# Performance work log

Hardware: AMD Instinct MI355X
Metric: run time of the kernel (lower is better)

The kernel has to match this reference:

```python
import jax, jax.numpy as jnp
import numpy as np

N_NODES = {'movie': 50000, 'director': 10000, 'actor': 25000}
# relation name -> (src_type, dst_type, num_edges)
RELS = {'md': ('movie', 'director', 150000),
        'dm': ('director', 'movie', 150000),
        'ma': ('movie', 'actor', 300000),
        'am': ('actor', 'movie', 300000)}
F_IN, HID, HEADS, OUT = 1024, 256, 8, 4
HD = HID // HEADS  # 32 per-head dim


def setup_inputs() -> dict:
    key = jax.random.key(0)
    kit = iter(jax.random.split(key, 128))
    def nrm(shape, s):
        return jax.random.normal(next(kit), shape, jnp.float32) * s
    inp = {}
    for t, n in N_NODES.items():
        inp['x_' + t] = nrm((n, F_IN), 1.0)
    for rn, (st, dt, e) in RELS.items():
        inp['e_' + rn + '_src'] = jax.random.randint(next(kit), (e,), 0, N_NODES[st], dtype=jnp.int32)
        inp['e_' + rn + '_dst'] = jax.random.randint(next(kit), (e,), 0, N_NODES[dt], dtype=jnp.int32)
        inp['a_' + rn] = nrm((HEADS, HD, HD), 0.05)   # per-relation attention matrix
        inp['m_' + rn] = nrm((HEADS, HD, HD), 0.05)   # per-relation message matrix
        inp['p_' + rn] = jnp.ones((HEADS,), jnp.float32)  # relation priority
    for t in N_NODES:
        inp['W_in_' + t] = nrm((F_IN, HID), 0.02)
        inp['b_in_' + t] = jnp.zeros((HID,), jnp.float32)
        for nm in ('k', 'q', 'v'):
            inp['W' + nm + '_' + t] = nrm((HID, HID), 0.05)
            inp['b' + nm + '_' + t] = jnp.zeros((HID,), jnp.float32)
        inp['Wa_' + t] = nrm((HID, HID), 0.05)
        inp['ba_' + t] = jnp.zeros((HID,), jnp.float32)
        inp['skip_' + t] = jnp.array(1.0, jnp.float32)
    inp['W_out'] = nrm((HID, OUT), 0.05)
    inp['b_out'] = jnp.zeros((OUT,), jnp.float32)
    return inp


def _forward(p):
    # per-node-type input projection (the HGT.lin_dict step)
    h = {t: p['x_' + t] @ p['W_in_' + t] + p['b_in_' + t] for t in N_NODES}
    # per-type K/Q/V projections, reshaped to [N, H, D]
    def proj(nm):
        return {t: (h[t] @ p['W' + nm + '_' + t] + p['b' + nm + '_' + t]).reshape(-1, HEADS, HD)
                for t in N_NODES}
    k, q, v = proj('k'), proj('q'), proj('v')
    scale = 1.0 / np.sqrt(HD)
    # per-edge-type: gather, relation-transform, score
    buf = {t: [] for t in N_NODES}
    for rn, (st, dt, _) in RELS.items():
        si, di = p['e_' + rn + '_src'], p['e_' + rn + '_dst']
        ke = jnp.einsum('ehd,hdf->ehf', k[st][si], p['a_' + rn])  # [E,H,D]
        ve = jnp.einsum('ehd,hdf->ehf', v[st][si], p['m_' + rn])  # [E,H,D]
        al = (q[dt][di] * ke).sum(-1) * (p['p_' + rn] * scale)    # [E,H]
        buf[dt].append((di, al, ve))
    # destination-grouped segment softmax + scatter aggregation
    out = {}
    for t, n in N_NODES.items():
        di = jnp.concatenate([b[0] for b in buf[t]])
        al = jnp.concatenate([b[1] for b in buf[t]])
        ve = jnp.concatenate([b[2] for b in buf[t]])
        amax = jax.ops.segment_max(al, di, num_segments=n)        # [N,H]
        amax = jnp.where(jnp.isfinite(amax), amax, 0.0)
        ex = jnp.exp(al - amax[di])
        den = jax.ops.segment_sum(ex, di, num_segments=n)[di]
        w = ex / jnp.where(den > 0, den, 1.0)                     # [E,H]
        agg = jax.ops.segment_sum(w[:, :, None] * ve, di, num_segments=n).reshape(n, HID)
        o = jax.nn.gelu(agg @ p['Wa_' + t] + p['ba_' + t])
        beta = jax.nn.sigmoid(p['skip_' + t])                     # gated skip connection
        out[t] = beta * o + (1.0 - beta) * h[t]
    # final classifier on movie nodes
    return out['movie'] @ p['W_out'] + p['b_out']


def reference(x_movie, x_director, x_actor, e_md_src, e_md_dst, a_md, m_md, p_md, e_dm_src, e_dm_dst, a_dm, m_dm, p_dm, e_ma_src, e_ma_dst, a_ma, m_ma, p_ma, e_am_src, e_am_dst, a_am, m_am, p_am, W_in_movie, b_in_movie, Wk_movie, bk_movie, Wq_movie, bq_movie, Wv_movie, bv_movie, Wa_movie, ba_movie, skip_movie, W_in_director, b_in_director, Wk_director, bk_director, Wq_director, bq_director, Wv_director, bv_director, Wa_director, ba_director, skip_director, W_in_actor, b_in_actor, Wk_actor, bk_actor, Wq_actor, bq_actor, Wv_actor, bv_actor, Wa_actor, ba_actor, skip_actor, W_out, b_out):
    p = dict(locals())
    return _forward(p)
```

## Files before the change

kernel.cpp:

```cpp
#include <hip/hip_runtime.h>
#include <math.h>

#define NM 50000
#define ND 10000
#define NA 25000
#define E_DM 150000
#define E_AM 300000
#define E_TOT (E_DM + E_AM)
#define HID 256
#define HEADS 8
#define HD 32
#define FIN 1024
#define SCALE 0.17677669529663687f

typedef __attribute__((ext_vector_type(8))) short short8;
typedef __attribute__((ext_vector_type(4))) float f32x4;

typedef __attribute__((address_space(1))) const unsigned char gas_u8;
typedef __attribute__((address_space(3))) unsigned char las_u8;

__device__ __forceinline__ void gload16(const void* g, void* l) {
    gas_u8* gp = (gas_u8*)(unsigned long long)(uintptr_t)g;
    las_u8* lp = (las_u8*)(unsigned int)(uintptr_t)l;
    __builtin_amdgcn_global_load_lds((const __attribute__((address_space(1))) void*)gp,
                                     (__attribute__((address_space(3))) void*)lp, 16, 0, 0);
}

__device__ __forceinline__ unsigned int pk_bf16(float x, float y) {
    unsigned int a = __float_as_uint(x), b = __float_as_uint(y);
    a += 0x7FFFu + ((a >> 16) & 1u);
    b += 0x7FFFu + ((b >> 16) & 1u);
    return (a >> 16) | (b & 0xFFFF0000u);
}
__device__ __forceinline__ unsigned short to_bf16(float x) {
    unsigned int a = __float_as_uint(x);
    a += 0x7FFFu + ((a >> 16) & 1u);
    return (unsigned short)(a >> 16);
}
__device__ __forceinline__ float bf2f(unsigned short u) {
    return __uint_as_float(((unsigned int)u) << 16);
}

struct F4 { const float* W[4]; const float* b[4]; const float* a[4]; float* Wf[4]; float* bf[4]; };
__global__ void fold_w4(F4 f4) {
    int di = blockIdx.y;
    const float* W = f4.W[di]; const float* b = f4.b[di]; const float* a = f4.a[di];
    float* Wf = f4.Wf[di]; float* bf = f4.bf[di];
    int c = threadIdx.x;
    int h = c >> 5, f = c & 31;
    int r = blockIdx.x;
    float acc = 0.f;
    if (r < HID) {
        #pragma unroll
        for (int d = 0; d < HD; ++d)
            acc += W[r * HID + h * HD + d] * a[(h * HD + d) * HD + f];
        Wf[r * HID + c] = acc;
    } else {
        #pragma unroll
        for (int d = 0; d < HD; ++d)
            acc += b[h * HD + d] * a[(h * HD + d) * HD + f];
        bf[c] = acc;
    }
}

struct PDesc { const float* W; unsigned short* out; int K; int b0; };
struct PMulti { PDesc d[9]; int nd; };
__global__ void wt_pack(PMulti pm) {
    int bid = blockIdx.x; int di = 0;
    #pragma unroll
    for (int i = 1; i < 9; ++i) if (i < pm.nd && bid >= pm.d[i].b0) di = i;
    PDesc p = pm.d[di];
    int kstep = bid - p.b0;
    int t = threadIdx.x;
    #pragma unroll
    for (int i = 0; i < 32; ++i) {
        int idx = i * 256 + t;
        int n0 = idx >> 9, r = idx & 511, lane = r >> 3, j = r & 7;
        int k = kstep * 32 + (lane >> 4) * 8 + j;
        int c = n0 * 16 + (lane & 15);
        p.out[(size_t)kstep * 8192 + idx] = to_bf16(p.W[(size_t)k * HID + c]);
    }
}

struct GDesc {
    const void* A; const unsigned short* Bt; const float* bias; void* C;
    const void* hskip; const float* gate; int M; int K; int epi; int obf; int abf; int b0;
};
struct GMulti { GDesc d[5]; int nd; };

#define GBM 64

__launch_bounds__(512, 6)
__global__ void gemm_mfma(GMulti mu) {
    __shared__ unsigned short sB[2][16 * 512];
    __shared__ unsigned short sA[2][4 * 512];

    int bid = blockIdx.x;
    int di = 0;
    #pragma unroll
    for (int i = 1; i < 5; ++i)
        if (i < mu.nd && bid >= mu.d[i].b0) di = i;
    GDesc g = mu.d[di];
    int bm = (bid - g.b0) * GBM;
    int M = g.M, K = g.K;

    int t = threadIdx.x;
    int lane = t & 63;
    int w = t >> 6;
    int wp = w >> 1;
    int ch = w & 1;
    int l16 = lane & 15;

    int slot = t >> 1;
    int ss_ = slot >> 6;
    int sl  = slot & 63;
    int arow_f = bm + ss_ * 16 + (sl & 15);
    int ak0    = (sl >> 4) * 8 + (t & 1) * 4;
    const float* Ap = nullptr;
    const unsigned short* Abp = nullptr;
    if (g.abf) {
        if (w < 4) {
            int r = bm + w * 16 + l16;
            Abp = (const unsigned short*)g.A + (size_t)min(r, M - 1) * K + ((lane >> 4) * 8);
        }
    } else {
        Ap = (const float*)g.A + (size_t)min(arow_f, M - 1) * K + ak0;
    }

    f32x4 acc[8];
    #pragma unroll
    for (int n = 0; n < 8; ++n) acc[n] = (f32x4)(0.f);

    int nk = K >> 5;
    {
        const unsigned short* gB = g.Bt;
        gload16(gB + w * 512 + lane * 8, &sB[0][w * 512]);
        gload16(gB + (w + 8) * 512 + lane * 8, &sB[0][(w + 8) * 512]);
        if (g.abf) {
            if (w < 4) gload16(Abp, &sA[0][w * 512]);
        } else {
            float4 f = *(const float4*)(Ap);
            uint2 pk = make_uint2(pk_bf16(f.x, f.y), pk_bf16(f.z, f.w));
            *(uint2*)&sA[0][slot * 8 + (t & 1) * 4] = pk;
        }
    }
    __syncthreads();

    int cur = 0;
    for (int ks = 0; ks < nk; ++ks) {
        int nxt = cur ^ 1;
        bool pf = (ks + 1 < nk);
        float4 f;
        if (pf) {
            const unsigned short* gB = g.Bt + (size_t)(ks + 1) * 8192;
            gload16(gB + w * 512 + lane * 8, &sB[nxt][w * 512]);
            gload16(gB + (w + 8) * 512 + lane * 8, &sB[nxt][(w + 8) * 512]);
            if (g.abf) {
                if (w < 4) gload16(Abp + (ks + 1) * 32, &sA[nxt][w * 512]);
            } else {
                f = *(const float4*)(Ap + (ks + 1) * 32);
            }
        }
        short8 af = *(const short8*)&sA[cur][(wp * 64 + lane) * 8];
        short8 bfr[8];
        #pragma unroll
        for (int n = 0; n < 8; ++n)
            bfr[n] = *(const short8*)&sB[cur][((ch * 8 + n) * 64 + lane) * 8];
        #pragma unroll
        for (int n = 0; n < 8; ++n)
            acc[n] = __builtin_amdgcn_mfma_f32_16x16x32_bf16(af, bfr[n], acc[n], 0, 0, 0);
        if (pf && !g.abf) {
            uint2 pk = make_uint2(pk_bf16(f.x, f.y), pk_bf16(f.z, f.w));
            *(uint2*)&sA[nxt][slot * 8 + (t & 1) * 4] = pk;
        }
        __syncthreads();
        cur = nxt;
    }

    float beta = 0.f;
    if (g.epi) beta = 1.f / (1.f + expf(-g.gate[0]));
    int r0 = bm + wp * 16 + ((lane >> 4) << 2);
    #pragma unroll
    for (int n = 0; n < 8; ++n) {
        int col = ch * 128 + n * 16 + l16;
        #pragma unroll
        for (int j = 0; j < 4; ++j) {
            int grow = r0 + j;
            if (grow >= M) continue;
            float v = acc[n][j] + g.bias[col];
            if (g.epi) {
                float x = v;
                float gl = 0.5f * x * (1.f + tanhf(0.7978845608028654f * (x + 0.044715f * x * x * x)));
                float hv = bf2f(((const unsigned short*)g.hskip)[(size_t)grow * HID + col]);
                v = beta * gl + (1.f - beta) * hv;
            }
            if (g.obf) ((unsigned short*)g.C)[(size_t)grow * HID + col] = to_bf16(v);
            else ((float*)g.C)[(size_t)grow * HID + col] = v;
        }
    }
}

__global__ void hist_deg(const int* __restrict__ dA, const int* __restrict__ dB,
                         int* __restrict__ deg) {
    int i = blockIdx.x * 256 + threadIdx.x;
    if (i < E_DM) atomicAdd(&deg[dA[i]], 1);
    else if (i < E_TOT) atomicAdd(&deg[dB[i - E_DM]], 1);
}

__global__ void scan_pass1(const int* __restrict__ deg, int* __restrict__ bsum) {
    __shared__ int s[256];
    int b = blockIdx.x, t = threadIdx.x;
    int i = b * 256 + t;
    int v = (i < NM) ? deg[i] : 0;
    s[t] = v; __syncthreads();
    for (int off = 128; off > 0; off >>= 1) {
        if (t < off) s[t] += s[t + off];
        __syncthreads();
    }
    if (t == 0) bsum[b] = s[0];
}

__global__ void scan_pass2(const int* __restrict__ bsum, int* __restrict__ boff, int nb) {
    __shared__ int s[256];
    int t = threadIdx.x;
    int v = (t < nb) ? bsum[t] : 0;
    s[t] = v; __syncthreads();
    for (int off = 1; off < 256; off <<= 1) {
        int x = (t >= off) ? s[t - off] : 0;
        __syncthreads();
        s[t] += x;
        __syncthreads();
    }
    if (t < nb) boff[t] = s[t] - v;
}

__global__ void scan_pass3(const int* __restrict__ deg, const int* __restrict__ boff,
                           int* __restrict__ rowptr, int* __restrict__ cursor) {
    __shared__ int s[256];
    int b = blockIdx.x, t = threadIdx.x, i = b * 256 + t;
    int v = (i < NM) ? deg[i] : 0;
    s[t] = v; __syncthreads();
    for (int off = 1; off < 256; off <<= 1) {
        int x = (t >= off) ? s[t - off] : 0;
        __syncthreads();
        s[t] += x;
        __syncthreads();
    }
    int excl = s[t] - v + boff[b];
    if (i < NM) { rowptr[i] = excl; cursor[i] = excl; }
    if (i == 0) rowptr[NM] = E_TOT;
}

__global__ void fill_adj(const int* __restrict__ sA, const int* __restrict__ dA,
                         const int* __restrict__ sB, const int* __restrict__ dB,
                         int* __restrict__ cursor, int* __restrict__ adj) {
    int i = blockIdx.x * 256 + threadIdx.x;
    int d, entry;
    if (i < E_DM)      { d = dA[i];        entry = sA[i]; }
    else if (i < E_TOT){ int j = i - E_DM; d = dB[j]; entry = (sB[j] + ND) | (1 << 16); }
    else return;
    int pos = atomicAdd(&cursor[d], 1);
    adj[pos] = entry;
}

__launch_bounds__(256)
__global__ void agg_fused(const int* __restrict__ rowptr, const int* __restrict__ adj,
                          const float* __restrict__ q, const unsigned short* __restrict__ kt_all,
                          const unsigned short* __restrict__ vt_all,
                          const float* __restrict__ p_dm, const float* __restrict__ p_am,
                          float* __restrict__ agg) {
    int d = blockIdx.x * 4 + (threadIdx.x >> 6);
    if (d >= NM) return;
    int lane = threadIdx.x & 63;
    int h = lane >> 3;
    int start = rowptr[d], end = rowptr[d + 1];
    float4 qv = *(const float4*)(q + (size_t)d * HID + lane * 4);
    float pr0 = p_dm[h] * SCALE, pr1 = p_am[h] * SCALE;
    float m = -INFINITY, den = 0.f, a0 = 0.f, a1 = 0.f, a2 = 0.f, a3 = 0.f;
    for (int i = start; i < end; ++i) {
        int e = adj[i];
        int sr = e & 0xFFFF;
        uint2 ku = *(const uint2*)(kt_all + (size_t)sr * HID + lane * 4);
        float k0 = __uint_as_float(ku.x << 16), k1 = __uint_as_float(ku.x & 0xFFFF0000u);
        float k2 = __uint_as_float(ku.y << 16), k3 = __uint_as_float(ku.y & 0xFFFF0000u);
        float prod = qv.x * k0 + qv.y * k1 + qv.z * k2 + qv.w * k3;
        prod += __shfl_xor(prod, 1);
        prod += __shfl_xor(prod, 2);
        prod += __shfl_xor(prod, 4);
        float a = prod * ((e >> 16) ? pr1 : pr0);
        float mn = fmaxf(m, a);
        float c  = __expf(m - mn);
        float ex = __expf(a - mn);
        uint2 vu = *(const uint2*)(vt_all + (size_t)sr * HID + lane * 4);
        float v0 = __uint_as_float(vu.x << 16), v1 = __uint_as_float(vu.x & 0xFFFF0000u);
        float v2 = __uint_as_float(vu.y << 16), v3 = __uint_as_float(vu.y & 0xFFFF0000u);
        den = den * c + ex;
        a0 = a0 * c + ex * v0; a1 = a1 * c + ex * v1;
        a2 = a2 * c + ex * v2; a3 = a3 * c + ex * v3;
        m = mn;
    }
    float inv = (end > start) ? 1.f / den : 0.f;
    *(float4*)(agg + (size_t)d * HID + lane * 4) = make_float4(a0 * inv, a1 * inv, a2 * inv, a3 * inv);
}

__launch_bounds__(256)
__global__ void classifier(const float* __restrict__ X, const float* __restrict__ W,
                           const float* __restrict__ b, float* __restrict__ out, int M) {
    int t = threadIdx.x, lane = t & 63;
    int wid = blockIdx.x * 4 + (t >> 6);
    int nw = gridDim.x * 4;
    float w0[4], w1[4], w2[4], w3[4];
    #pragma unroll
    for (int j = 0; j < 4; ++j) {
        float4 wv = *(const float4*)(W + (lane * 4 + j) * 4);
        w0[j] = wv.x; w1[j] = wv.y; w2[j] = wv.z; w3[j] = wv.w;
    }
    float b0 = b[0], b1 = b[1], b2 = b[2], b3 = b[3];
    for (int row = wid; row < M; row += nw) {
        float4 x = *(const float4*)(X + (size_t)row * HID + lane * 4);
        float s0 = x.x * w0[0] + x.y * w0[1] + x.z * w0[2] + x.w * w0[3];
        float s1 = x.x * w1[0] + x.y * w1[1] + x.z * w1[2] + x.w * w1[3];
        float s2 = x.x * w2[0] + x.y * w2[1] + x.z * w2[2] + x.w * w2[3];
        float s3 = x.x * w3[0] + x.y * w3[1] + x.z * w3[2] + x.w * w3[3];
        #pragma unroll
        for (int off = 32; off > 0; off >>= 1) {
            s0 += __shfl_xor(s0, off); s1 += __shfl_xor(s1, off);
            s2 += __shfl_xor(s2, off); s3 += __shfl_xor(s3, off);
        }
        if (lane == 0) {
            float4 o = make_float4(s0 + b0, s1 + b1, s2 + b2, s3 + b3);
            *(float4*)(out + (size_t)row * 4) = o;
        }
    }
}

extern "C" void kernel_launch(void* const* d_in, const int* in_sizes, int n_in,
                              void* d_out, int out_size, void* d_ws, size_t ws_size,
                              hipStream_t stream) {
    (void)in_sizes; (void)n_in; (void)out_size; (void)ws_size;
    const float* x_movie    = (const float*)d_in[0];
    const float* x_director = (const float*)d_in[1];
    const float* x_actor    = (const float*)d_in[2];
    const int*   e_dm_src = (const int*)d_in[8];
    const int*   e_dm_dst = (const int*)d_in[9];
    const float* a_dm     = (const float*)d_in[10];
    const float* m_dm     = (const float*)d_in[11];
    const float* p_dm     = (const float*)d_in[12];
    const int*   e_am_src = (const int*)d_in[18];
    const int*   e_am_dst = (const int*)d_in[19];
    const float* a_am     = (const float*)d_in[20];
    const float* m_am     = (const float*)d_in[21];
    const float* p_am     = (const float*)d_in[22];
    const float* W_in_m = (const float*)d_in[23];
    const float* b_in_m = (const float*)d_in[24];
    const float* Wq_m   = (const float*)d_in[27];
    const float* bq_m   = (const float*)d_in[28];
    const float* Wa_m   = (const float*)d_in[31];
    const float* ba_m   = (const float*)d_in[32];
    const float* skip_m = (const float*)d_in[33];
    const float* W_in_d = (const float*)d_in[34];
    const float* b_in_d = (const float*)d_in[35];
    const float* Wk_d   = (const float*)d_in[36];
    const float* bk_d   = (const float*)d_in[37];
    const float* Wv_d   = (const float*)d_in[40];
    const float* bv_d   = (const float*)d_in[41];
    const float* W_in_a = (const float*)d_in[45];
    const float* b_in_a = (const float*)d_in[46];
    const float* Wk_a   = (const float*)d_in[47];
    const float* bk_a   = (const float*)d_in[48];
    const float* Wv_a   = (const float*)d_in[51];
    const float* bv_a   = (const float*)d_in[52];
    const float* W_out  = (const float*)d_in[56];
    const float* b_out  = (const float*)d_in[57];

    char* base = (char*)d_ws;
    size_t off = 0;
    auto alloc = [&](size_t bytes) -> void* {
        void* p = base + off;
        off = (off + bytes + 255) & ~(size_t)255;
        return p;
    };
    unsigned short* h_m = (unsigned short*)alloc((size_t)NM * HID * 2);
    unsigned short* h_d = (unsigned short*)alloc((size_t)ND * HID * 2);
    unsigned short* h_a = (unsigned short*)alloc((size_t)NA * HID * 2);
    float* q_m    = (float*)alloc((size_t)NM * HID * 4);
    float* out_m  = (float*)alloc((size_t)NM * HID * 4);
    float* agg    = (float*)alloc((size_t)NM * HID * 4);
    unsigned short* kt_all = (unsigned short*)alloc((size_t)(ND + NA) * HID * 2);
    unsigned short* vt_all = (unsigned short*)alloc((size_t)(ND + NA) * HID * 2);
    float* Wf     = (float*)alloc(4 * (size_t)HID * HID * 4);
    float* bf     = (float*)alloc(4 * (size_t)HID * 4);
    int* deg      = (int*)alloc(NM * 4);
    int* rowptr   = (int*)alloc((NM + 1) * 4);
    int* cursor   = (int*)alloc(NM * 4);
    int* bsum     = (int*)alloc(256 * 4);
    int* boff     = (int*)alloc(256 * 4);
    int* adj      = (int*)alloc((size_t)E_TOT * 4);
    unsigned short* Bt_in_m = (unsigned short*)alloc((size_t)256 * 1024 * 2);
    unsigned short* Bt_in_d = (unsigned short*)alloc((size_t)256 * 1024 * 2);
    unsigned short* Bt_in_a = (unsigned short*)alloc((size_t)256 * 1024 * 2);
    unsigned short* Bt_q_m  = (unsigned short*)alloc((size_t)256 * 256 * 2);
    unsigned short* Bt_k_dm = (unsigned short*)alloc((size_t)256 * 256 * 2);
    unsigned short* Bt_v_dm = (unsigned short*)alloc((size_t)256 * 256 * 2);
    unsigned short* Bt_k_am = (unsigned short*)alloc((size_t)256 * 256 * 2);
    unsigned short* Bt_v_am = (unsigned short*)alloc((size_t)256 * 256 * 2);
    unsigned short* Bt_a_m  = (unsigned short*)alloc((size_t)256 * 256 * 2);

    unsigned short* kt_dm = kt_all;
    unsigned short* kt_am = kt_all + (size_t)ND * HID;
    unsigned short* vt_dm = vt_all;
    unsigned short* vt_am = vt_all + (size_t)ND * HID;

    float* Wf_k_dm = Wf + 0 * HID * HID;  float* bf_k_dm = bf + 0 * HID;
    float* Wf_v_dm = Wf + 1 * HID * HID;  float* bf_v_dm = bf + 1 * HID;
    float* Wf_k_am = Wf + 2 * HID * HID;  float* bf_k_am = bf + 2 * HID;
    float* Wf_v_am = Wf + 3 * HID * HID;  float* bf_v_am = bf + 3 * HID;

    hipMemsetAsync(deg, 0, NM * sizeof(int), stream);
    hist_deg<<<(E_TOT + 255) / 256, 256, 0, stream>>>(e_dm_dst, e_am_dst, deg);
    int nb = (NM + 255) / 256;
    scan_pass1<<<nb, 256, 0, stream>>>(deg, bsum);
    scan_pass2<<<1, 256, 0, stream>>>(bsum, boff, nb);
    scan_pass3<<<nb, 256, 0, stream>>>(deg, boff, rowptr, cursor);
    fill_adj<<<(E_TOT + 255) / 256, 256, 0, stream>>>(e_dm_src, e_dm_dst, e_am_src, e_am_dst,
                                                      cursor, adj);

    {
        F4 f4{};
        f4.W[0] = Wk_d; f4.b[0] = bk_d; f4.a[0] = a_dm; f4.Wf[0] = Wf_k_dm; f4.bf[0] = bf_k_dm;
        f4.W[1] = Wv_d; f4.b[1] = bv_d; f4.a[1] = m_dm; f4.Wf[1] = Wf_v_dm; f4.bf[1] = bf_v_dm;
        f4.W[2] = Wk_a; f4.b[2] = bk_a; f4.a[2] = a_am; f4.Wf[2] = Wf_k_am; f4.bf[2] = bf_k_am;
        f4.W[3] = Wv_a; f4.b[3] = bv_a; f4.a[3] = m_am; f4.Wf[3] = Wf_v_am; f4.bf[3] = bf_v_am;
        fold_w4<<<dim3(257, 4), 256, 0, stream>>>(f4);
    }
    {
        PMulti pm{};
        pm.nd = 9;
        int b0 = 0;
        pm.d[0] = {W_in_m,  Bt_in_m, FIN, b0}; b0 += 32;
        pm.d[1] = {W_in_d,  Bt_in_d, FIN, b0}; b0 += 32;
        pm.d[2] = {W_in_a,  Bt_in_a, FIN, b0}; b0 += 32;
        pm.d[3] = {Wq_m,    Bt_q_m,  HID, b0}; b0 += 8;
        pm.d[4] = {Wf_k_dm, Bt_k_dm, HID, b0}; b0 += 8;
        pm.d[5] = {Wf_v_dm, Bt_v_dm, HID, b0}; b0 += 8;
        pm.d[6] = {Wf_k_am, Bt_k_am, HID, b0}; b0 += 8;
        pm.d[7] = {Wf_v_am, Bt_v_am, HID, b0}; b0 += 8;
        pm.d[8] = {Wa_m,    Bt_a_m,  HID, b0}; b0 += 8;
        wt_pack<<<b0, 256, 0, stream>>>(pm);
    }

    int bm_m = (NM + GBM - 1) / GBM;
    int bm_d = (ND + GBM - 1) / GBM;
    int bm_a = (NA + GBM - 1) / GBM;

    {
        GMulti mu{};
        mu.nd = 3;
        mu.d[0] = {x_movie,    Bt_in_m, b_in_m, h_m, nullptr, nullptr, NM, FIN, 0, 1, 0, 0};
        mu.d[1] = {x_director, Bt_in_d, b_in_d, h_d, nullptr, nullptr, ND, FIN, 0, 1, 0, bm_m};
        mu.d[2] = {x_actor,    Bt_in_a, b_in_a, h_a, nullptr, nullptr, NA, FIN, 0, 1, 0, bm_m + bm_d};
        gemm_mfma<<<bm_m + bm_d + bm_a, 512, 0, stream>>>(mu);
    }
    {
        GMulti mu{};
        mu.nd = 5;
        int b0 = 0;
        mu.d[0] = {h_m, Bt_q_m,  bq_m,    q_m,   nullptr, nullptr, NM, HID, 0, 0, 1, b0}; b0 += bm_m;
        mu.d[1] = {h_d, Bt_k_dm, bf_k_dm, kt_dm, nullptr, nullptr, ND, HID, 0, 1, 1, b0}; b0 += bm_d;
        mu.d[2] = {h_d, Bt_v_dm, bf_v_dm, vt_dm, nullptr, nullptr, ND, HID, 0, 1, 1, b0}; b0 += bm_d;
        mu.d[3] = {h_a, Bt_k_am, bf_k_am, kt_am, nullptr, nullptr, NA, HID, 0, 1, 1, b0}; b0 += bm_a;
        mu.d[4] = {h_a, Bt_v_am, bf_v_am, vt_am, nullptr, nullptr, NA, HID, 0, 1, 1, b0}; b0 += bm_a;
        gemm_mfma<<<b0, 512, 0, stream>>>(mu);
    }

    agg_fused<<<(NM + 3) / 4, 256, 0, stream>>>(rowptr, adj, q_m, kt_all, vt_all, p_dm, p_am, agg);

    {
        GMulti mu{};
        mu.nd = 1;
        mu.d[0] = {agg, Bt_a_m, ba_m, out_m, h_m, skip_m, NM, HID, 1, 0, 0, 0};
        gemm_mfma<<<bm_m, 512, 0, stream>>>(mu);
    }

    classifier<<<256, 256, 0, stream>>>(out_m, W_out, b_out, (float*)d_out, NM);
}
```

Before: 416.7 us.

## Split GEMM tiles into column halves and store q/agg in bf16

The GEMM kernel now launches 256-thread blocks, and each block computes one 128-column half of a 64-row tile, so there are twice as many blocks with half the B shared-memory footprint. The fp32 A-load path is reorganised so each thread converts eight floats. The q projection and the aggregation output are now written as bf16, which halves their memory traffic and lets the output GEMM take bf16 A through the direct global-to-LDS load path. In exchange, the A tile is loaded twice (once per column half) and q and agg lose precision.

```diff
diff --git a/kernel.cpp b/kernel.cpp
--- a/kernel.cpp
+++ b/kernel.cpp
@@ -90,9 +90,9 @@
 
 #define GBM 64
 
-__launch_bounds__(512, 6)
+__launch_bounds__(256, 6)
 __global__ void gemm_mfma(GMulti mu) {
-    __shared__ unsigned short sB[2][16 * 512];
+    __shared__ unsigned short sB[2][8 * 512];
     __shared__ unsigned short sA[2][4 * 512];
 
     int bid = blockIdx.x;
@@ -101,31 +101,26 @@
     for (int i = 1; i < 5; ++i)
         if (i < mu.nd && bid >= mu.d[i].b0) di = i;
     GDesc g = mu.d[di];
-    int bm = (bid - g.b0) * GBM;
+    int bid2 = bid - g.b0;
+    int bm = (bid2 >> 1) * GBM;
+    int chb = bid2 & 1;
     int M = g.M, K = g.K;
 
     int t = threadIdx.x;
     int lane = t & 63;
     int w = t >> 6;
-    int wp = w >> 1;
-    int ch = w & 1;
     int l16 = lane & 15;
 
-    int slot = t >> 1;
-    int ss_ = slot >> 6;
-    int sl  = slot & 63;
-    int arow_f = bm + ss_ * 16 + (sl & 15);
-    int ak0    = (sl >> 4) * 8 + (t & 1) * 4;
     const float* Ap = nullptr;
     const unsigned short* Abp = nullptr;
     if (g.abf) {
-        if (w < 4) {
-            int r = bm + w * 16 + l16;
-            Abp = (const unsigned short*)g.A + (size_t)min(r, M - 1) * K + ((lane >> 4) * 8);
-        }
+        int r = bm + w * 16 + l16;
+        Abp = (const unsigned short*)g.A + (size_t)min(r, M - 1) * K + ((lane >> 4) * 8);
     } else {
-        Ap = (const float*)g.A + (size_t)min(arow_f, M - 1) * K + ak0;
-    }
+        int arow = bm + w * 16 + (t & 15);
+        Ap = (const float*)g.A + (size_t)min(arow, M - 1) * K + (((t >> 4) & 3) * 8);
+    }
+    const unsigned short* gBb = g.Bt + (size_t)(chb * 8) * 512;
 
     f32x4 acc[8];
     #pragma unroll
@@ -133,15 +128,18 @@
 
     int nk = K >> 5;
     {
-        const unsigned short* gB = g.Bt;
-        gload16(gB + w * 512 + lane * 8, &sB[0][w * 512]);
-        gload16(gB + (w + 8) * 512 + lane * 8, &sB[0][(w + 8) * 512]);
+        #pragma unroll
+        for (int i = 0; i < 2; ++i) {
+            int s = w * 2 + i;
+            gload16(gBb + s * 512 + lane * 8, &sB[0][s * 512]);
+        }
         if (g.abf) {
-            if (w < 4) gload16(Abp, &sA[0][w * 512]);
+            gload16(Abp, &sA[0][w * 512]);
         } else {
-            float4 f = *(const float4*)(Ap);
-            uint2 pk = make_uint2(pk_bf16(f.x, f.y), pk_bf16(f.z, f.w));
-            *(uint2*)&sA[0][slot * 8 + (t & 1) * 4] = pk;
+            float4 f0 = *(const float4*)(Ap);
+            float4 f1 = *(const float4*)(Ap + 4);
+            *(uint4*)&sA[0][t * 8] = make_uint4(pk_bf16(f0.x, f0.y), pk_bf16(f0.z, f0.w),
+                                                pk_bf16(f1.x, f1.y), pk_bf16(f1.z, f1.w));
         }
     }
     __syncthreads();
@@ -150,28 +148,30 @@
     for (int ks = 0; ks < nk; ++ks) {
         int nxt = cur ^ 1;
         bool pf = (ks + 1 < nk);
-        float4 f;
+        float4 f0, f1;
         if (pf) {
-            const unsigned short* gB = g.Bt + (size_t)(ks + 1) * 8192;
-            gload16(gB + w * 512 + lane * 8, &sB[nxt][w * 512]);
-            gload16(gB + (w + 8) * 512 + lane * 8, &sB[nxt][(w + 8) * 512]);
+            const unsigned short* gB = gBb + (size_t)(ks + 1) * 8192;
+            #pragma unroll
+            for (int i = 0; i < 2; ++i) {
+                int s = w * 2 + i;
+                gload16(gB + s * 512 + lane * 8, &sB[nxt][s * 512]);
+            }
             if (g.abf) {
-                if (w < 4) gload16(Abp + (ks + 1) * 32, &sA[nxt][w * 512]);
+                gload16(Abp + (ks + 1) * 32, &sA[nxt][w * 512]);
             } else {
-                f = *(const float4*)(Ap + (ks + 1) * 32);
+                f0 = *(const float4*)(Ap + (ks + 1) * 32);
+                f1 = *(const float4*)(Ap + (ks + 1) * 32 + 4);
             }
         }
-        short8 af = *(const short8*)&sA[cur][(wp * 64 + lane) * 8];
-        short8 bfr[8];
-        #pragma unroll
-        for (int n = 0; n < 8; ++n)
-            bfr[n] = *(const short8*)&sB[cur][((ch * 8 + n) * 64 + lane) * 8];
-        #pragma unroll
-        for (int n = 0; n < 8; ++n)
-            acc[n] = __builtin_amdgcn_mfma_f32_16x16x32_bf16(af, bfr[n], acc[n], 0, 0, 0);
+        short8 af = *(const short8*)&sA[cur][w * 512 + lane * 8];
+        #pragma unroll
+        for (int n = 0; n < 8; ++n) {
+            short8 bfr = *(const short8*)&sB[cur][n * 512 + lane * 8];
+            acc[n] = __builtin_amdgcn_mfma_f32_16x16x32_bf16(af, bfr, acc[n], 0, 0, 0);
+        }
         if (pf && !g.abf) {
-            uint2 pk = make_uint2(pk_bf16(f.x, f.y), pk_bf16(f.z, f.w));
-            *(uint2*)&sA[nxt][slot * 8 + (t & 1) * 4] = pk;
+            *(uint4*)&sA[nxt][t * 8] = make_uint4(pk_bf16(f0.x, f0.y), pk_bf16(f0.z, f0.w),
+                                                  pk_bf16(f1.x, f1.y), pk_bf16(f1.z, f1.w));
         }
         __syncthreads();
         cur = nxt;
@@ -179,10 +179,10 @@
 
     float beta = 0.f;
     if (g.epi) beta = 1.f / (1.f + expf(-g.gate[0]));
-    int r0 = bm + wp * 16 + ((lane >> 4) << 2);
+    int r0 = bm + w * 16 + ((lane >> 4) << 2);
     #pragma unroll
     for (int n = 0; n < 8; ++n) {
-        int col = ch * 128 + n * 16 + l16;
+        int col = chb * 128 + n * 16 + l16;
         #pragma unroll
         for (int j = 0; j < 4; ++j) {
             int grow = r0 + j;
@@ -265,16 +265,18 @@
 
 __launch_bounds__(256)
 __global__ void agg_fused(const int* __restrict__ rowptr, const int* __restrict__ adj,
-                          const float* __restrict__ q, const unsigned short* __restrict__ kt_all,
+                          const unsigned short* __restrict__ q, const unsigned short* __restrict__ kt_all,
                           const unsigned short* __restrict__ vt_all,
                           const float* __restrict__ p_dm, const float* __restrict__ p_am,
-                          float* __restrict__ agg) {
+                          unsigned short* __restrict__ agg) {
     int d = blockIdx.x * 4 + (threadIdx.x >> 6);
     if (d >= NM) return;
     int lane = threadIdx.x & 63;
     int h = lane >> 3;
     int start = rowptr[d], end = rowptr[d + 1];
-    float4 qv = *(const float4*)(q + (size_t)d * HID + lane * 4);
+    uint2 qu = *(const uint2*)(q + (size_t)d * HID + lane * 4);
+    float q0 = __uint_as_float(qu.x << 16), q1 = __uint_as_float(qu.x & 0xFFFF0000u);
+    float q2 = __uint_as_float(qu.y << 16), q3 = __uint_as_float(qu.y & 0xFFFF0000u);
     float pr0 = p_dm[h] * SCALE, pr1 = p_am[h] * SCALE;
     float m = -INFINITY, den = 0.f, a0 = 0.f, a1 = 0.f, a2 = 0.f, a3 = 0.f;
     for (int i = start; i < end; ++i) {
@@ -283,7 +285,7 @@
         uint2 ku = *(const uint2*)(kt_all + (size_t)sr * HID + lane * 4);
         float k0 = __uint_as_float(ku.x << 16), k1 = __uint_as_float(ku.x & 0xFFFF0000u);
         float k2 = __uint_as_float(ku.y << 16), k3 = __uint_as_float(ku.y & 0xFFFF0000u);
-        float prod = qv.x * k0 + qv.y * k1 + qv.z * k2 + qv.w * k3;
+        float prod = q0 * k0 + q1 * k1 + q2 * k2 + q3 * k3;
         prod += __shfl_xor(prod, 1);
         prod += __shfl_xor(prod, 2);
         prod += __shfl_xor(prod, 4);
@@ -300,7 +302,8 @@
         m = mn;
     }
     float inv = (end > start) ? 1.f / den : 0.f;
-    *(float4*)(agg + (size_t)d * HID + lane * 4) = make_float4(a0 * inv, a1 * inv, a2 * inv, a3 * inv);
+    *(uint2*)(agg + (size_t)d * HID + lane * 4) =
+        make_uint2(pk_bf16(a0 * inv, a1 * inv), pk_bf16(a2 * inv, a3 * inv));
 }
 
 __launch_bounds__(256)
@@ -383,9 +386,9 @@
     unsigned short* h_m = (unsigned short*)alloc((size_t)NM * HID * 2);
     unsigned short* h_d = (unsigned short*)alloc((size_t)ND * HID * 2);
     unsigned short* h_a = (unsigned short*)alloc((size_t)NA * HID * 2);
-    float* q_m    = (float*)alloc((size_t)NM * HID * 4);
+    unsigned short* q_m = (unsigned short*)alloc((size_t)NM * HID * 2);
     float* out_m  = (float*)alloc((size_t)NM * HID * 4);
-    float* agg    = (float*)alloc((size_t)NM * HID * 4);
+    unsigned short* agg = (unsigned short*)alloc((size_t)NM * HID * 2);
     unsigned short* kt_all = (unsigned short*)alloc((size_t)(ND + NA) * HID * 2);
     unsigned short* vt_all = (unsigned short*)alloc((size_t)(ND + NA) * HID * 2);
     float* Wf     = (float*)alloc(4 * (size_t)HID * HID * 4);
@@ -457,20 +460,20 @@
         GMulti mu{};
         mu.nd = 3;
         mu.d[0] = {x_movie,    Bt_in_m, b_in_m, h_m, nullptr, nullptr, NM, FIN, 0, 1, 0, 0};
-        mu.d[1] = {x_director, Bt_in_d, b_in_d, h_d, nullptr, nullptr, ND, FIN, 0, 1, 0, bm_m};
-        mu.d[2] = {x_actor,    Bt_in_a, b_in_a, h_a, nullptr, nullptr, NA, FIN, 0, 1, 0, bm_m + bm_d};
-        gemm_mfma<<<bm_m + bm_d + bm_a, 512, 0, stream>>>(mu);
+        mu.d[1] = {x_director, Bt_in_d, b_in_d, h_d, nullptr, nullptr, ND, FIN, 0, 1, 0, bm_m * 2};
+        mu.d[2] = {x_actor,    Bt_in_a, b_in_a, h_a, nullptr, nullptr, NA, FIN, 0, 1, 0, (bm_m + bm_d) * 2};
+        gemm_mfma<<<(bm_m + bm_d + bm_a) * 2, 256, 0, stream>>>(mu);
     }
     {
         GMulti mu{};
         mu.nd = 5;
         int b0 = 0;
-        mu.d[0] = {h_m, Bt_q_m,  bq_m,    q_m,   nullptr, nullptr, NM, HID, 0, 0, 1, b0}; b0 += bm_m;
-        mu.d[1] = {h_d, Bt_k_dm, bf_k_dm, kt_dm, nullptr, nullptr, ND, HID, 0, 1, 1, b0}; b0 += bm_d;
-        mu.d[2] = {h_d, Bt_v_dm, bf_v_dm, vt_dm, nullptr, nullptr, ND, HID, 0, 1, 1, b0}; b0 += bm_d;
-        mu.d[3] = {h_a, Bt_k_am, bf_k_am, kt_am, nullptr, nullptr, NA, HID, 0, 1, 1, b0}; b0 += bm_a;
-        mu.d[4] = {h_a, Bt_v_am, bf_v_am, vt_am, nullptr, nullptr, NA, HID, 0, 1, 1, b0}; b0 += bm_a;
-        gemm_mfma<<<b0, 512, 0, stream>>>(mu);
+        mu.d[0] = {h_m, Bt_q_m,  bq_m,    q_m,   nullptr, nullptr, NM, HID, 0, 1, 1, b0}; b0 += bm_m * 2;
+        mu.d[1] = {h_d, Bt_k_dm, bf_k_dm, kt_dm, nullptr, nullptr, ND, HID, 0, 1, 1, b0}; b0 += bm_d * 2;
+        mu.d[2] = {h_d, Bt_v_dm, bf_v_dm, vt_dm, nullptr, nullptr, ND, HID, 0, 1, 1, b0}; b0 += bm_d * 2;
+        mu.d[3] = {h_a, Bt_k_am, bf_k_am, kt_am, nullptr, nullptr, NA, HID, 0, 1, 1, b0}; b0 += bm_a * 2;
+        mu.d[4] = {h_a, Bt_v_am, bf_v_am, vt_am, nullptr, nullptr, NA, HID, 0, 1, 1, b0}; b0 += bm_a * 2;
+        gemm_mfma<<<b0, 256, 0, stream>>>(mu);
     }
 
     agg_fused<<<(NM + 3) / 4, 256, 0, stream>>>(rowptr, adj, q_m, kt_all, vt_all, p_dm, p_am, agg);
@@ -478,8 +481,8 @@
     {
         GMulti mu{};
         mu.nd = 1;
-        mu.d[0] = {agg, Bt_a_m, ba_m, out_m, h_m, skip_m, NM, HID, 1, 0, 0, 0};
-        gemm_mfma<<<bm_m, 512, 0, stream>>>(mu);
+        mu.d[0] = {agg, Bt_a_m, ba_m, out_m, h_m, skip_m, NM, HID, 1, 0, 1, 0};
+        gemm_mfma<<<bm_m * 2, 256, 0, stream>>>(mu);
     }
 
     classifier<<<256, 256, 0, stream>>>(out_m, W_out, b_out, (float*)d_out, NM);
```

Result: slower. 444.0 us (+6.6%).
